# Optimization experiments

Hardware: AMD Instinct MI355X
Metric: run time of the kernel (lower is better)

## Reference

```python
import jax, jax.numpy as jnp
import numpy as np

B, N_VIS, N_TXT = 2, 2048, 256
N_HEAD, HEAD_DIM = 16, 64
C = N_HEAD * HEAD_DIM  # 1024
EPS = 1e-6


def setup_inputs() -> dict:
    key = jax.random.key(0)
    ks = jax.random.split(key, 24)
    s = 0.02
    inp = {
        'vis_x': jax.random.normal(ks[0], (B, N_VIS, C), jnp.float32),
        'txt_x': jax.random.normal(ks[1], (B, N_TXT, C), jnp.float32),
        'rope_cos': jax.random.uniform(ks[2], (N_VIS, HEAD_DIM), jnp.float32, -1.0, 1.0),
        'rope_sin': jax.random.uniform(ks[3], (N_VIS, HEAD_DIM), jnp.float32, -1.0, 1.0),
    }
    names = ['vis_qw', 'vis_kw', 'vis_vw', 'vis_ow', 'txt_qw', 'txt_kw', 'txt_vw', 'txt_ow']
    for i, n in enumerate(names):
        inp[n] = jax.random.normal(ks[4 + i], (C, C), jnp.float32) * s
        inp[n[:-1] + 'b'] = jnp.zeros((C,), jnp.float32)
    for n in ['vis_qn', 'vis_kn', 'txt_qn', 'txt_kn']:
        inp[n] = jnp.ones((HEAD_DIM,), jnp.float32)
    return inp


def _heads(x, w, b):
    # x: [B,N,C] -> [B,H,N,D]  (torch Linear: x @ W.T + b)
    y = x @ w.T + b
    Bn, N, _ = y.shape
    return y.reshape(Bn, N, N_HEAD, HEAD_DIM).transpose(0, 2, 1, 3)


def _rmsnorm(x, g):
    return x * jax.lax.rsqrt(jnp.mean(x * x, axis=-1, keepdims=True) + EPS) * g


def _rope(x, cos, sin):
    # interleaved-pair rotation: pairs (x0,x1) -> (-x1, x0)
    xr, xi = x[..., 0::2], x[..., 1::2]
    rot = jnp.stack([-xi, xr], axis=-1).reshape(x.shape)
    return x * cos[None, None] + rot * sin[None, None]


def reference(vis_x, txt_x, rope_cos, rope_sin,
              vis_qw, vis_qb, vis_kw, vis_kb, vis_vw, vis_vb, vis_ow, vis_ob,
              txt_qw, txt_qb, txt_kw, txt_kb, txt_vw, txt_vb, txt_ow, txt_ob,
              vis_qn, vis_kn, txt_qn, txt_kn):
    q_vis = _rmsnorm(_heads(vis_x, vis_qw, vis_qb), vis_qn)
    k_vis = _rmsnorm(_heads(vis_x, vis_kw, vis_kb), vis_kn)
    v_vis = _heads(vis_x, vis_vw, vis_vb)
    q_txt = _rmsnorm(_heads(txt_x, txt_qw, txt_qb), txt_qn)
    k_txt = _rmsnorm(_heads(txt_x, txt_kw, txt_kb), txt_kn)
    v_txt = _heads(txt_x, txt_vw, txt_vb)

    q_vis = _rope(q_vis, rope_cos, rope_sin)
    k_vis = _rope(k_vis, rope_cos, rope_sin)

    q = jnp.concatenate([q_txt, q_vis], axis=2)  # [B,H,S,D]
    k = jnp.concatenate([k_txt, k_vis], axis=2)
    v = jnp.concatenate([v_txt, v_vis], axis=2)

    scale = 1.0 / jnp.sqrt(jnp.asarray(HEAD_DIM, q.dtype))
    scores = jnp.einsum('bhqd,bhkd->bhqk', q, k) * scale
    attn = jax.nn.softmax(scores, axis=-1)
    out = jnp.einsum('bhqk,bhkd->bhqd', attn, v)  # [B,H,S,D]

    txt_out = out[:, :, :N_TXT, :].transpose(0, 2, 1, 3).reshape(q.shape[0], N_TXT, C)
    vis_out = out[:, :, N_TXT:, :].transpose(0, 2, 1, 3).reshape(q.shape[0], N_VIS, C)
    vis_out = vis_out @ vis_ow.T + vis_ob
    txt_out = txt_out @ txt_ow.T + txt_ob
    return (vis_out, txt_out)
```

## Files before the change

### kernel.cpp

```cpp
#include <hip/hip_runtime.h>

typedef _Float16 h8 __attribute__((ext_vector_type(8)));
typedef _Float16 h4 __attribute__((ext_vector_type(4)));
typedef _Float16 h2 __attribute__((ext_vector_type(2)));
typedef float f4 __attribute__((ext_vector_type(4)));
typedef float f16x16 __attribute__((ext_vector_type(16)));

#define LOG2E 1.44269504088896340736f

#define BARRIER_ACQ do { __builtin_amdgcn_s_barrier(); \
                         asm volatile("" ::: "memory"); } while (0)
#define BARRIER_REL do { asm volatile("" ::: "memory"); \
                         __builtin_amdgcn_s_barrier(); } while (0)

__device__ __forceinline__ void gload_lds16(const void* g, void* l) {
    __builtin_amdgcn_global_load_lds(
        (const __attribute__((address_space(1))) void*)g,
        (__attribute__((address_space(3))) void*)l, 16, 0, 0);
}

struct CastArgs { const float* src[10]; _Float16* dst[10]; };

__global__ __launch_bounds__(256) void cast_all_kernel(CastArgs a) {
    int blk = blockIdx.x;
    int seg, rel;
    if (blk < 4096)      { seg = 0; rel = blk; }
    else if (blk < 4608) { seg = 1; rel = blk - 4096; }
    else { int t = blk - 4608; seg = 2 + (t >> 10); rel = t & 1023; }
    long base = ((long)rel * 256 + threadIdx.x) * 4;
    float4 v = *(const float4*)(a.src[seg] + base);
    h4 o = { (_Float16)v.x, (_Float16)v.y, (_Float16)v.z, (_Float16)v.w };
    *(h4*)(a.dst[seg] + base) = o;
}

struct GemmDesc {
    const _Float16* A[2];
    const _Float16* W[2];
    char*           C[2];
    const float*    bias[2][3];
    long bsA[2];
    long aoff[2];
    long bsC[2];
    int  mshift[2];
    int  mcut;
};

template<bool OUT_F32>
__global__ __launch_bounds__(256)
void gemm_kernel(GemmDesc g, int K, int N, int gm, int gn, int xgn)
{
    __shared__ __align__(16) _Float16 As[2][128 * 64];
    __shared__ __align__(16) _Float16 Bs[2][128 * 64];
    const int lane = threadIdx.x & 63;
    const int wave = threadIdx.x >> 6;
    const int lid = blockIdx.x;
    const int xcd = lid & 7;
    const int r0 = lid >> 3;
    const int mtile = (xcd / xgn) * gm + (r0 % gm);
    const int ntile = (xcd % xgn) * gn + (r0 / gm);

    const int seg = mtile >= g.mcut;
    const int mloc = mtile - (seg ? g.mcut : 0);
    const int bidx = mloc >> g.mshift[seg];
    const int min_ = mloc & ((1 << g.mshift[seg]) - 1);
    const _Float16* Ab = g.A[seg] + (long)bidx * g.bsA[seg] + g.aoff[seg]
                         + (long)min_ * 128 * K;
    const _Float16* Bb = g.W[seg] + (long)ntile * 128 * K;
    const long crow0 = (long)bidx * g.bsC[seg] + (long)min_ * 128 * N;

    const int wr = wave >> 1, wc = wave & 1;
    f4 acc[4][4] = {};

    auto stage = [&](int bf, int kt) {
#pragma unroll
        for (int it = 0; it < 4; ++it) {
            int r = wave * 32 + it * 8 + (lane >> 3);
            int lc = (lane & 7) ^ (r & 7);
            gload_lds16((const char*)(Ab + (long)r * K + kt) + lc * 16,
                        (char*)&As[bf][0] + (wave * 32 + it * 8) * 128);
            gload_lds16((const char*)(Bb + (long)r * K + kt) + lc * 16,
                        (char*)&Bs[bf][0] + (wave * 32 + it * 8) * 128);
        }
    };

    const int nk = K >> 6;
    stage(0, 0);
    int buf = 0;
#pragma unroll 1
    for (int ki = 0; ki < nk; ++ki) {
        if (ki + 1 < nk) {
            stage(buf ^ 1, (ki + 1) << 6);
            asm volatile("s_waitcnt vmcnt(8)" ::: "memory");
        } else {
            asm volatile("s_waitcnt vmcnt(0)" ::: "memory");
        }
        BARRIER_ACQ;
#pragma unroll
        for (int kk = 0; kk < 2; ++kk) {
            h8 af[4], bf4[4];
#pragma unroll
            for (int m = 0; m < 4; ++m) {
                int row = wr * 64 + m * 16 + (lane & 15);
                int pc = (kk * 4 + (lane >> 4)) ^ (row & 7);
                af[m] = *(const h8*)(&As[buf][row * 64 + pc * 8]);
            }
#pragma unroll
            for (int n = 0; n < 4; ++n) {
                int row = wc * 64 + n * 16 + (lane & 15);
                int pc = (kk * 4 + (lane >> 4)) ^ (row & 7);
                bf4[n] = *(const h8*)(&Bs[buf][row * 64 + pc * 8]);
            }
#pragma unroll
            for (int m = 0; m < 4; ++m)
#pragma unroll
                for (int n = 0; n < 4; ++n)
                    acc[m][n] = __builtin_amdgcn_mfma_f32_16x16x32_f16(
                        af[m], bf4[n], acc[m][n], 0, 0, 0);
        }
        BARRIER_REL;
        buf ^= 1;
    }

#pragma unroll
    for (int n = 0; n < 4; ++n) {
        int col = ntile * 128 + wc * 64 + n * 16 + (lane & 15);
        const float* bp = (col < 1024) ? g.bias[seg][0]
                        : (col < 2048) ? g.bias[seg][1] : g.bias[seg][2];
        float bv = bp[col & 1023];
#pragma unroll
        for (int m = 0; m < 4; ++m) {
            int lrow = wr * 64 + m * 16 + ((lane >> 4) << 2);
#pragma unroll
            for (int r = 0; r < 4; ++r) {
                float v = acc[m][n][r] + bv;
                long off = crow0 + (long)(lrow + r) * N + col;
                if (OUT_F32) ((float*)g.C[seg])[off] = v;
                else         ((_Float16*)g.C[seg])[off] = (_Float16)v;
            }
        }
    }
}

__device__ __forceinline__ float ssum8(h8 v) {
    float s = 0.f;
#pragma unroll
    for (int j = 0; j < 8; ++j) { float f = (float)v[j]; s += f * f; }
    return s;
}
__device__ __forceinline__ float red8(float s) {
    s += __shfl_xor(s, 1); s += __shfl_xor(s, 2); s += __shfl_xor(s, 4);
    return s;
}
__device__ __forceinline__ h8 norm_rope(h8 v, float rs_, const float* g, float gmul,
                                        const float* cs, const float* sn, int vis) {
    float f[8];
#pragma unroll
    for (int j = 0; j < 8; ++j) f[j] = (float)v[j] * rs_ * g[j] * gmul;
    h8 o;
    if (vis) {
#pragma unroll
        for (int j = 0; j < 8; j += 2) {
            float a = f[j], b = f[j + 1];
            o[j]     = (_Float16)(a * cs[j]     - b * sn[j]);
            o[j + 1] = (_Float16)(b * cs[j + 1] + a * sn[j + 1]);
        }
    } else {
#pragma unroll
        for (int j = 0; j < 8; ++j) o[j] = (_Float16)f[j];
    }
    return o;
}

__global__ __launch_bounds__(256)
void pass2_kernel(const _Float16* __restrict__ Yv, const _Float16* __restrict__ Yt,
                  const float* __restrict__ gqv, const float* __restrict__ gkv_,
                  const float* __restrict__ gqt, const float* __restrict__ gkt,
                  const float* __restrict__ rc, const float* __restrict__ rs,
                  _Float16* __restrict__ Q, _Float16* __restrict__ Kd)
{
    const int wave = threadIdx.x >> 6;
    const int lane = threadIdx.x & 63;
    const int row = blockIdx.x * 4 + wave;
    const int is_vis = row < 4096;
    const _Float16* y;
    const float *gq, *gk;
    int b, n, npos;
    if (is_vis) {
        y = Yv + (long)row * 3072; gq = gqv; gk = gkv_;
        b = row >> 11; n = row & 2047; npos = 256 + n;
    } else {
        int r2 = row - 4096;
        y = Yt + (long)r2 * 3072; gq = gqt; gk = gkt;
        b = r2 >> 8; n = r2 & 255; npos = n;
    }
    const int h0 = lane >> 3;
    const int d0 = (lane & 7) * 8;

    h8 q0 = *(const h8*)(y + lane * 8);
    h8 q1 = *(const h8*)(y + 512 + lane * 8);
    h8 k0 = *(const h8*)(y + 1024 + lane * 8);
    h8 k1 = *(const h8*)(y + 1536 + lane * 8);

    float ga[8], gb[8];
    *(float4*)(ga)     = *(const float4*)(gq + d0);
    *(float4*)(ga + 4) = *(const float4*)(gq + d0 + 4);
    *(float4*)(gb)     = *(const float4*)(gk + d0);
    *(float4*)(gb + 4) = *(const float4*)(gk + d0 + 4);
    float cs[8], sn[8];
    if (is_vis) {
        *(float4*)(cs)     = *(const float4*)(rc + n * 64 + d0);
        *(float4*)(cs + 4) = *(const float4*)(rc + n * 64 + d0 + 4);
        *(float4*)(sn)     = *(const float4*)(rs + n * 64 + d0);
        *(float4*)(sn + 4) = *(const float4*)(rs + n * 64 + d0 + 4);
    }

    const float rq0 = rsqrtf(red8(ssum8(q0)) * (1.0f / 64.0f) + 1e-6f);
    const float rq1 = rsqrtf(red8(ssum8(q1)) * (1.0f / 64.0f) + 1e-6f);
    const float rk0 = rsqrtf(red8(ssum8(k0)) * (1.0f / 64.0f) + 1e-6f);
    const float rk1 = rsqrtf(red8(ssum8(k1)) * (1.0f / 64.0f) + 1e-6f);

    const float qmul = 0.125f * LOG2E;
    const long obA = (((long)b * 16 + h0)      * 2304 + npos) * 64 + d0;
    const long obB = (((long)b * 16 + h0 + 8)  * 2304 + npos) * 64 + d0;
    *(h8*)(Q + obA)  = norm_rope(q0, rq0, ga, qmul, cs, sn, is_vis);
    *(h8*)(Q + obB)  = norm_rope(q1, rq1, ga, qmul, cs, sn, is_vis);
    *(h8*)(Kd + obA) = norm_rope(k0, rk0, gb, 1.0f, cs, sn, is_vis);
    *(h8*)(Kd + obB) = norm_rope(k1, rk1, gb, 1.0f, cs, sn, is_vis);
}

__global__ __launch_bounds__(256)
void vtrans_kernel(const _Float16* __restrict__ Yv, const _Float16* __restrict__ Yt,
                   _Float16* __restrict__ Vt)
{
    __shared__ _Float16 T[64 * 136];
    const int blk = blockIdx.x;
    const int bh = blk / 18, ntl = blk - bh * 18;
    const int b = bh >> 4, h = bh & 15;
    const int npos0 = ntl * 128;
    const _Float16* Y; long m0;
    if (ntl >= 2) { Y = Yv; m0 = (long)b * 2048 + (npos0 - 256); }
    else          { Y = Yt; m0 = (long)b * 256 + npos0; }
    const int t = threadIdx.x;
    const _Float16* src = Y + m0 * 3072 + 2048 + h * 64;
#pragma unroll
    for (int ri = 0; ri < 4; ++ri) {
        int row = ri * 32 + (t >> 3);
        int c8 = t & 7;
        h8 v = *(const h8*)(src + (long)row * 3072 + c8 * 8);
#pragma unroll
        for (int j = 0; j < 8; ++j)
            T[(c8 * 8 + j) * 136 + row] = v[j];
    }
    __syncthreads();
    const int d = t >> 2, ch = t & 3;
    _Float16* dst = Vt + ((long)bh * 64 + d) * 2304 + npos0 + ch * 32;
#pragma unroll
    for (int k = 0; k < 4; ++k)
        *(h8*)(dst + k * 8) = *(const h8*)(&T[d * 136 + ch * 32 + k * 8]);
}

__device__ __forceinline__ void attn_stage(const char* Kt, const char* Vt, char* S,
                                           int bufB, int t,
                                           int gK0, int gK1, int gV0, int gV1,
                                           int ldsW) {
    const char* kt = Kt + (long)t * 8192;
    const char* vt = Vt + (long)t * 128;
    gload_lds16(kt + gK0, S + bufB + ldsW);
    gload_lds16(kt + gK1, S + bufB + 4096 + ldsW);
    gload_lds16(vt + gV0, S + 16384 + bufB + ldsW);
    gload_lds16(vt + gV1, S + 16384 + bufB + 4096 + ldsW);
}

__device__ __forceinline__ void pv_half(const float* p, const char* S, int vbase,
                                        const int* off, int kblk,
                                        f16x16* oacc, float& psum) {
    const h2 one2 = {(_Float16)1.f, (_Float16)1.f};
#pragma unroll
    for (int kb = 0; kb < 2; ++kb) {
        unsigned w0 = __builtin_bit_cast(unsigned,
            __builtin_amdgcn_cvt_pkrtz(p[8 * kb + 0], p[8 * kb + 1]));
        unsigned w1 = __builtin_bit_cast(unsigned,
            __builtin_amdgcn_cvt_pkrtz(p[8 * kb + 2], p[8 * kb + 3]));
        unsigned w2 = __builtin_bit_cast(unsigned,
            __builtin_amdgcn_cvt_pkrtz(p[8 * kb + 4], p[8 * kb + 5]));
        unsigned w3 = __builtin_bit_cast(unsigned,
            __builtin_amdgcn_cvt_pkrtz(p[8 * kb + 6], p[8 * kb + 7]));
        psum = __builtin_amdgcn_fdot2(__builtin_bit_cast(h2, w0), one2, psum, false);
        psum = __builtin_amdgcn_fdot2(__builtin_bit_cast(h2, w1), one2, psum, false);
        psum = __builtin_amdgcn_fdot2(__builtin_bit_cast(h2, w2), one2, psum, false);
        psum = __builtin_amdgcn_fdot2(__builtin_bit_cast(h2, w3), one2, psum, false);
        asm("v_permlane32_swap_b32 %0, %1" : "+v"(w0), "+v"(w2));
        asm("v_permlane32_swap_b32 %0, %1" : "+v"(w1), "+v"(w3));
        union { unsigned u[4]; h8 v; } pa;
        pa.u[0] = w0; pa.u[1] = w1; pa.u[2] = w2; pa.u[3] = w3;
#pragma unroll
        for (int dblk = 0; dblk < 2; ++dblk) {
            h8 vb = *(const h8*)(S + vbase + dblk * 4096 + off[kblk * 2 + kb]);
            oacc[dblk] = __builtin_amdgcn_mfma_f32_32x32x16_f16(
                pa.v, vb, oacc[dblk], 0, 0, 0);
        }
    }
}

__device__ __forceinline__ void attn_tile(const char* S, int bufB, const int* off,
                                          const h8* qf, f16x16* oacc, float& psum) {
    const f16x16 kZero = {};
    f16x16 st0, st1;
    {
        h8 ka0 = *(const h8*)(S + bufB + off[0]);
        h8 ka1 = *(const h8*)(S + bufB + 4096 + off[0]);
        st0 = __builtin_amdgcn_mfma_f32_32x32x16_f16(ka0, qf[0], kZero, 0, 0, 0);
        st1 = __builtin_amdgcn_mfma_f32_32x32x16_f16(ka1, qf[0], kZero, 0, 0, 0);
    }
#pragma unroll
    for (int ds = 1; ds < 4; ++ds) {
        h8 ka0 = *(const h8*)(S + bufB + off[ds]);
        h8 ka1 = *(const h8*)(S + bufB + 4096 + off[ds]);
        st0 = __builtin_amdgcn_mfma_f32_32x32x16_f16(ka0, qf[ds], st0, 0, 0, 0);
        st1 = __builtin_amdgcn_mfma_f32_32x32x16_f16(ka1, qf[ds], st1, 0, 0, 0);
    }
    float p0[16], p1[16];
#pragma unroll
    for (int r = 0; r < 16; ++r) { p0[r] = exp2f(st0[r]); p1[r] = exp2f(st1[r]); }
    pv_half(p0, S, 16384 + bufB, off, 0, oacc, psum);
    pv_half(p1, S, 16384 + bufB, off, 1, oacc, psum);
}

__global__ __launch_bounds__(256, 4)
void attn_kernel(const _Float16* __restrict__ Qg,
                 const _Float16* __restrict__ Kg,
                 const _Float16* __restrict__ Vg,
                 _Float16* __restrict__ Op,
                 float* __restrict__ Lp,
                 int nt, int cpx)
{
    __shared__ __align__(16) char S[32768];
    const int lane = threadIdx.x & 63;
    const int wave = threadIdx.x >> 6;
    const int l31 = lane & 31, hi = lane >> 5;
    const int d0 = blockIdx.x;
    const int id = (d0 & 7) * cpx + (d0 >> 3);
    const int split = id / 576;
    const int rem = id - split * 576;
    const int bh = rem / 18;
    const int qb = rem - bh * 18;
    const int b = bh >> 4, h = bh & 15;
    const _Float16* Qbh = Qg + (long)bh * 2304 * 64;
    const char* Kt = (const char*)(Kg + (long)bh * 2304 * 64) + (long)split * nt * 8192;
    const char* Vt = (const char*)(Vg + (long)bh * 64 * 2304) + (long)split * nt * 128;
    _Float16* Ops = Op + (long)split * 4718592;
    float* Lps = Lp + (long)split * 73728;
    const int q0 = qb * 128 + wave * 32;

    h8 qf[4];
#pragma unroll
    for (int ds = 0; ds < 4; ++ds)
        qf[ds] = *(const h8*)(Qbh + (long)(q0 + l31) * 64 + ds * 16 + hi * 8);

    const int sg16 = ((lane & 7) ^ (lane >> 3)) * 16;
    const int rK = wave * 8 + (lane >> 3);
    const int gK0 = rK * 128 + sg16;
    const int gK1 = gK0 + 32 * 128;
    const int gV0 = rK * 4608 + sg16;
    const int gV1 = gV0 + 32 * 4608;
    const int ldsW = wave * 1024;
    int off[4];
#pragma unroll
    for (int j = 0; j < 4; ++j)
        off[j] = l31 * 128 + (((j * 2 + hi) ^ (l31 & 7)) * 16);

    f16x16 oacc[2] = {};
    float psum = 0.f;

    attn_stage(Kt, Vt, S, 0, 0, gK0, gK1, gV0, gV1, ldsW);
    int buf = 0;
#pragma unroll 1
    for (int t = 0; t < nt; ++t) {
        if (t + 1 < nt) {
            attn_stage(Kt, Vt, S, (buf ^ 1) * 8192, t + 1, gK0, gK1, gV0, gV1, ldsW);
            asm volatile("s_waitcnt vmcnt(4)" ::: "memory");
        } else {
            asm volatile("s_waitcnt vmcnt(0)" ::: "memory");
        }
        BARRIER_ACQ;
        __builtin_amdgcn_s_setprio(1);
        attn_tile(S, buf * 8192, off, qf, oacc, psum);
        __builtin_amdgcn_s_setprio(0);
        BARRIER_REL;
        buf ^= 1;
    }

    float lsum = psum + __shfl_xor(psum, 32);
    if (hi == 0) Lps[(long)bh * 2304 + q0 + l31] = lsum;
#pragma unroll
    for (int dblk = 0; dblk < 2; ++dblk) {
        int dcol = h * 64 + dblk * 32 + l31;
#pragma unroll
        for (int r = 0; r < 16; ++r) {
            int qrow = q0 + (r & 3) + 8 * (r >> 2) + 4 * hi;
            Ops[((long)b * 2304 + qrow) * 1024 + dcol] = (_Float16)oacc[dblk][r];
        }
    }
}

__global__ __launch_bounds__(256)
void combine_kernel(const _Float16* __restrict__ Op,
                    const float* __restrict__ Lp,
                    _Float16* __restrict__ Oh, int ns)
{
    long i = ((long)blockIdx.x * 256 + threadIdx.x) * 8;
    long row = i >> 10;
    int bb = row >= 2304;
    int n = (int)row - bb * 2304;
    int h = ((int)i & 1023) >> 6;
    long lidx = ((long)(bb * 16 + h)) * 2304 + n;
    float l = 0.f;
    float acc[8] = {};
    for (int s = 0; s < ns; ++s) {
        l += Lp[(long)s * 73728 + lidx];
        h8 a = *(const h8*)(Op + (long)s * 4718592 + i);
#pragma unroll
        for (int j = 0; j < 8; ++j) acc[j] += (float)a[j];
    }
    float inv = 1.0f / l;
    h8 o;
#pragma unroll
    for (int j = 0; j < 8; ++j) o[j] = (_Float16)(acc[j] * inv);
    *(h8*)(Oh + i) = o;
}

extern "C" void kernel_launch(void* const* d_in, const int* in_sizes, int n_in,
                              void* d_out, int out_size, void* d_ws, size_t ws_size,
                              hipStream_t stream)
{
    const float* vis_x    = (const float*)d_in[0];
    const float* txt_x    = (const float*)d_in[1];
    const float* rope_cos = (const float*)d_in[2];
    const float* rope_sin = (const float*)d_in[3];
    const float* vis_qw = (const float*)d_in[4];
    const float* vis_qb = (const float*)d_in[5];
    const float* vis_kw = (const float*)d_in[6];
    const float* vis_kb = (const float*)d_in[7];
    const float* vis_vw = (const float*)d_in[8];
    const float* vis_vb = (const float*)d_in[9];
    const float* vis_ow = (const float*)d_in[10];
    const float* vis_ob = (const float*)d_in[11];
    const float* txt_qw = (const float*)d_in[12];
    const float* txt_qb = (const float*)d_in[13];
    const float* txt_kw = (const float*)d_in[14];
    const float* txt_kb = (const float*)d_in[15];
    const float* txt_vw = (const float*)d_in[16];
    const float* txt_vb = (const float*)d_in[17];
    const float* txt_ow = (const float*)d_in[18];
    const float* txt_ob = (const float*)d_in[19];
    const float* vis_qn = (const float*)d_in[20];
    const float* vis_kn = (const float*)d_in[21];
    const float* txt_qn = (const float*)d_in[22];
    const float* txt_kn = (const float*)d_in[23];

    char* ws = (char*)d_ws;
    _Float16* Xvis  = (_Float16*)(ws);
    _Float16* Xtxt  = (_Float16*)(ws + 8388608);
    _Float16* Qh    = (_Float16*)(ws);
    _Float16* WqkvV = (_Float16*)(ws + 9437184);
    _Float16* WqkvT = (_Float16*)(ws + 15728640);
    _Float16* WoV   = (_Float16*)(ws + 22020096);
    _Float16* WoT   = (_Float16*)(ws + 24117248);
    _Float16* Yvis  = (_Float16*)(ws + 26214400);
    _Float16* Ytxt  = (_Float16*)(ws + 51380224);
    _Float16* Kh    = (_Float16*)(ws + 54525952);
    _Float16* Vth   = (_Float16*)(ws + 63963136);

    const int ns = (ws_size >= 112328704) ? 4 : 2;
    const int nt = (ns == 4) ? 9 : 18;
    _Float16* OpP;
    if (ns == 4) OpP = (_Float16*)(ws + 73400320);
    else         OpP = (_Float16*)(ws + 26214400);
    float* LpP = (float*)((char*)OpP + (size_t)ns * 9437184);
    _Float16* Oh = OpP;

    CastArgs ca;
    ca.src[0] = vis_x;  ca.dst[0] = Xvis;
    ca.src[1] = txt_x;  ca.dst[1] = Xtxt;
    ca.src[2] = vis_qw; ca.dst[2] = WqkvV;
    ca.src[3] = vis_kw; ca.dst[3] = WqkvV + 1048576;
    ca.src[4] = vis_vw; ca.dst[4] = WqkvV + 2097152;
    ca.src[5] = txt_qw; ca.dst[5] = WqkvT;
    ca.src[6] = txt_kw; ca.dst[6] = WqkvT + 1048576;
    ca.src[7] = txt_vw; ca.dst[7] = WqkvT + 2097152;
    ca.src[8] = vis_ow; ca.dst[8] = WoV;
    ca.src[9] = txt_ow; ca.dst[9] = WoT;
    cast_all_kernel<<<12800, 256, 0, stream>>>(ca);

    GemmDesc gq;
    gq.A[0] = Xvis;  gq.A[1] = Xtxt;
    gq.W[0] = WqkvV; gq.W[1] = WqkvT;
    gq.C[0] = (char*)Yvis; gq.C[1] = (char*)Ytxt;
    gq.bias[0][0] = vis_qb; gq.bias[0][1] = vis_kb; gq.bias[0][2] = vis_vb;
    gq.bias[1][0] = txt_qb; gq.bias[1][1] = txt_kb; gq.bias[1][2] = txt_vb;
    gq.bsA[0] = 0; gq.bsA[1] = 0;
    gq.aoff[0] = 0; gq.aoff[1] = 0;
    gq.bsC[0] = 0; gq.bsC[1] = 0;
    gq.mshift[0] = 5; gq.mshift[1] = 5;
    gq.mcut = 32;
    gemm_kernel<false><<<864, 256, 0, stream>>>(gq, 1024, 3072, 9, 12, 2);

    pass2_kernel<<<1152, 256, 0, stream>>>(
        Yvis, Ytxt, vis_qn, vis_kn, txt_qn, txt_kn, rope_cos, rope_sin, Qh, Kh);
    vtrans_kernel<<<576, 256, 0, stream>>>(Yvis, Ytxt, Vth);

    attn_kernel<<<576 * ns, 256, 0, stream>>>(Qh, Kh, Vth, OpP, LpP, nt, 72 * ns);
    combine_kernel<<<2304, 256, 0, stream>>>(OpP, LpP, Oh, ns);

    GemmDesc go;
    go.A[0] = Oh; go.A[1] = Oh;
    go.W[0] = WoV; go.W[1] = WoT;
    go.C[0] = (char*)d_out; go.C[1] = (char*)((float*)d_out + 4194304);
    go.bias[0][0] = vis_ob; go.bias[0][1] = vis_ob; go.bias[0][2] = vis_ob;
    go.bias[1][0] = txt_ob; go.bias[1][1] = txt_ob; go.bias[1][2] = txt_ob;
    go.bsA[0] = 2359296;  go.bsA[1] = 2359296;
    go.aoff[0] = 262144;  go.aoff[1] = 0;
    go.bsC[0] = 2097152;  go.bsC[1] = 262144;
    go.mshift[0] = 4; go.mshift[1] = 1;
    go.mcut = 32;
    gemm_kernel<true><<<288, 256, 0, stream>>>(go, 1024, 1024, 9, 4, 2);
}
```

Baseline: 176.0 us.

## Use 512-thread attention blocks with 256 query rows sharing each K/V tile

Doubles the attention workgroup from 4 to 8 waves, so each block covers 256 query rows and each loaded K/V tile in LDS is reused by twice as many waves. Each thread now issues one K and one V global-to-LDS load per stage instead of two, which halves the per-thread load work and lowers the vmcnt wait. The barriers are wrapped in sched_barrier fences to stop the compiler moving instructions across them. In exchange, each barrier now synchronizes more waves, there are fewer blocks in the grid, and the occupancy hint changes to (512, 6).

Result: slower. 190.5 us (+8.3%).

```diff
diff --git a/kernel.cpp b/kernel.cpp
--- a/kernel.cpp
+++ b/kernel.cpp
@@ -12,6 +12,12 @@
                          asm volatile("" ::: "memory"); } while (0)
 #define BARRIER_REL do { asm volatile("" ::: "memory"); \
                          __builtin_amdgcn_s_barrier(); } while (0)
+
+#define BARH do { asm volatile("" ::: "memory"); \
+                  __builtin_amdgcn_sched_barrier(0); \
+                  __builtin_amdgcn_s_barrier(); \
+                  __builtin_amdgcn_sched_barrier(0); \
+                  asm volatile("" ::: "memory"); } while (0)
 
 __device__ __forceinline__ void gload_lds16(const void* g, void* l) {
     __builtin_amdgcn_global_load_lds(
@@ -260,15 +266,10 @@
 }
 
 __device__ __forceinline__ void attn_stage(const char* Kt, const char* Vt, char* S,
-                                           int bufB, int t,
-                                           int gK0, int gK1, int gV0, int gV1,
+                                           int bufB, int t, int gK, int gV,
                                            int ldsW) {
-    const char* kt = Kt + (long)t * 8192;
-    const char* vt = Vt + (long)t * 128;
-    gload_lds16(kt + gK0, S + bufB + ldsW);
-    gload_lds16(kt + gK1, S + bufB + 4096 + ldsW);
-    gload_lds16(vt + gV0, S + 16384 + bufB + ldsW);
-    gload_lds16(vt + gV1, S + 16384 + bufB + 4096 + ldsW);
+    gload_lds16(Kt + (long)t * 8192 + gK, S + bufB + ldsW);
+    gload_lds16(Vt + (long)t * 128 + gV, S + 16384 + bufB + ldsW);
 }
 
 __device__ __forceinline__ void pv_half(const float* p, const char* S, int vbase,
@@ -326,7 +327,7 @@
     pv_half(p1, S, 16384 + bufB, off, 1, oacc, psum);
 }
 
-__global__ __launch_bounds__(256, 4)
+__global__ __launch_bounds__(512, 6)
 void attn_kernel(const _Float16* __restrict__ Qg,
                  const _Float16* __restrict__ Kg,
                  const _Float16* __restrict__ Vg,
@@ -340,29 +341,26 @@
     const int l31 = lane & 31, hi = lane >> 5;
     const int d0 = blockIdx.x;
     const int id = (d0 & 7) * cpx + (d0 >> 3);
-    const int split = id / 576;
-    const int rem = id - split * 576;
-    const int bh = rem / 18;
-    const int qb = rem - bh * 18;
+    const int split = id / 288;
+    const int rem = id - split * 288;
+    const int bh = rem / 9;
+    const int qb = rem - bh * 9;
     const int b = bh >> 4, h = bh & 15;
     const _Float16* Qbh = Qg + (long)bh * 2304 * 64;
     const char* Kt = (const char*)(Kg + (long)bh * 2304 * 64) + (long)split * nt * 8192;
     const char* Vt = (const char*)(Vg + (long)bh * 64 * 2304) + (long)split * nt * 128;
     _Float16* Ops = Op + (long)split * 4718592;
     float* Lps = Lp + (long)split * 73728;
-    const int q0 = qb * 128 + wave * 32;
+    const int q0 = qb * 256 + wave * 32;
 
     h8 qf[4];
 #pragma unroll
     for (int ds = 0; ds < 4; ++ds)
         qf[ds] = *(const h8*)(Qbh + (long)(q0 + l31) * 64 + ds * 16 + hi * 8);
 
-    const int sg16 = ((lane & 7) ^ (lane >> 3)) * 16;
     const int rK = wave * 8 + (lane >> 3);
-    const int gK0 = rK * 128 + sg16;
-    const int gK1 = gK0 + 32 * 128;
-    const int gV0 = rK * 4608 + sg16;
-    const int gV1 = gV0 + 32 * 4608;
+    const int gK = rK * 128 + (((lane & 7) ^ (rK & 7)) * 16);
+    const int gV = rK * 4608 + (((lane & 7) ^ (rK & 7)) * 16);
     const int ldsW = wave * 1024;
     int off[4];
 #pragma unroll
@@ -372,21 +370,21 @@
     f16x16 oacc[2] = {};
     float psum = 0.f;
 
-    attn_stage(Kt, Vt, S, 0, 0, gK0, gK1, gV0, gV1, ldsW);
+    attn_stage(Kt, Vt, S, 0, 0, gK, gV, ldsW);
     int buf = 0;
 #pragma unroll 1
     for (int t = 0; t < nt; ++t) {
         if (t + 1 < nt) {
-            attn_stage(Kt, Vt, S, (buf ^ 1) * 8192, t + 1, gK0, gK1, gV0, gV1, ldsW);
-            asm volatile("s_waitcnt vmcnt(4)" ::: "memory");
+            attn_stage(Kt, Vt, S, (buf ^ 1) * 8192, t + 1, gK, gV, ldsW);
+            asm volatile("s_waitcnt vmcnt(2)" ::: "memory");
         } else {
             asm volatile("s_waitcnt vmcnt(0)" ::: "memory");
         }
-        BARRIER_ACQ;
+        BARH;
         __builtin_amdgcn_s_setprio(1);
         attn_tile(S, buf * 8192, off, qf, oacc, psum);
         __builtin_amdgcn_s_setprio(0);
-        BARRIER_REL;
+        BARH;
         buf ^= 1;
     }
 
@@ -509,7 +507,7 @@
         Yvis, Ytxt, vis_qn, vis_kn, txt_qn, txt_kn, rope_cos, rope_sin, Qh, Kh);
     vtrans_kernel<<<576, 256, 0, stream>>>(Yvis, Ytxt, Vth);
 
-    attn_kernel<<<576 * ns, 256, 0, stream>>>(Qh, Kh, Vth, OpP, LpP, nt, 72 * ns);
+    attn_kernel<<<288 * ns, 512, 0, stream>>>(Qh, Kh, Vth, OpP, LpP, nt, 36 * ns);
     combine_kernel<<<2304, 256, 0, stream>>>(OpP, LpP, Oh, ns);
 
     GemmDesc go;
```
